# Optimization experiments

Measured on AMD Instinct MI355X. Metric: run time of the kernel, lower is better.

## Reference

```python
import jax, jax.numpy as jnp
import numpy as np

N = 524288
D_LATENT = 64


def _euler_to_quaternion(e):
    # e: [N,3] (roll, pitch, yaw). Mirrors euler_to_quaternion; stack order [qx,qy,qz,qw].
    r, p, y = e[:, 0] * 0.5, e[:, 1] * 0.5, e[:, 2] * 0.5
    sr, cr = jnp.sin(r), jnp.cos(r)
    sp, cp = jnp.sin(p), jnp.cos(p)
    sy, cy = jnp.sin(y), jnp.cos(y)
    qx = sr * cp * cy - cr * sp * sy
    qy = cr * sp * cy + sr * cp * sy
    qz = cr * cp * sy - sr * sp * cy
    qw = cr * cp * cy + sr * sp * sy
    return jnp.stack([qx, qy, qz, qw], axis=-1)  # [N,4]


def _compute_rot_mats(rot):
    # rot: [N,3] azimuth/elevation/theta in radians. Mirrors compute_RotMats (degree=False).
    a = -rot[:, 0]
    e = jnp.pi / 2.0 + rot[:, 1]
    t = -rot[:, 2]
    sa, ca = jnp.sin(a), jnp.cos(a)
    se, ce = jnp.sin(e), jnp.cos(e)
    st, ct = jnp.sin(t), jnp.cos(t)
    z = jnp.zeros_like(a)
    o = jnp.ones_like(a)
    Rz = jnp.stack([jnp.stack([ca, -sa, z], -1),
                    jnp.stack([sa, ca, z], -1),
                    jnp.stack([z, z, o], -1)], -2)   # [N,3,3]
    Rx = jnp.stack([jnp.stack([o, z, z], -1),
                    jnp.stack([z, ce, -se], -1),
                    jnp.stack([z, se, ce], -1)], -2)
    Rz2 = jnp.stack([jnp.stack([ct, -st, z], -1),
                     jnp.stack([st, ct, z], -1),
                     jnp.stack([z, z, o], -1)], -2)
    return jnp.einsum('nij,njk,nkl->nil', Rz2, Rx, Rz)  # [N,3,3]


def setup_inputs() -> dict:
    key = jax.random.key(0)
    k = jax.random.split(key, 6)
    return {
        'pose_pred': jax.random.uniform(k[0], (N, 3), dtype=jnp.float32),
        'pose_gt': jax.random.uniform(k[1], (N, 3), dtype=jnp.float32),
        'trans_pred': jax.random.normal(k[2], (N, 3), dtype=jnp.float32),
        'trans_gt': jax.random.normal(k[3], (N, 3), dtype=jnp.float32),
        'latent_pred': jax.random.normal(k[4], (N, D_LATENT), dtype=jnp.float32),
        'latent_gt': jax.random.normal(k[5], (N, D_LATENT), dtype=jnp.float32),
    }


def reference(pose_pred, pose_gt, trans_pred, trans_gt, latent_pred, latent_gt):
    # category='laptop' -> symm=False (no zeroing of elevation column)
    pp = pose_pred * jnp.pi
    pg = pose_gt * jnp.pi

    # rot_loss: MSE between quaternions (compute_quat_loss)
    rot_loss = jnp.mean((_euler_to_quaternion(pp) - _euler_to_quaternion(pg)) ** 2)

    # trans_loss / latent_loss: plain MSE (compute_l2_loss)
    trans_loss = jnp.mean((trans_pred - trans_gt) ** 2)
    latent_loss = jnp.mean((latent_pred - latent_gt) ** 2)

    # rot_distance: geodesic angle in degrees (rot_error, fully vectorized over batch)
    Rp = _compute_rot_mats(pp)
    Rg = _compute_rot_mats(pg)
    tr = jnp.einsum('nij,nij->n', Rp, Rg)  # trace(Rp @ Rg^T)
    rot_distance = jnp.arccos(jnp.clip((tr - 1.0) * 0.5, -1.0, 1.0)) * (180.0 / jnp.pi)  # [N]

    # trans_distance (trans_error)
    tp = trans_pred[:, 0:1] * trans_pred[:, 1:3]
    tg = trans_gt[:, 0:1] * trans_gt[:, 1:3]
    trans_distance = jnp.linalg.norm(tg - tp, axis=1) * 100.0  # [N]

    return (rot_loss, trans_loss, latent_loss, rot_distance, trans_distance)
```

## Files before the change

kernel.cpp:

```cpp
#include <hip/hip_runtime.h>
#include <math.h>

constexpr int NROWS = 524288;
constexpr float PI_F = 3.14159265358979323846f;
constexpr int BLOCK = 256;
constexpr int PA_BLOCKS = 512;
constexpr int TOTAL_BLOCKS = 2048;
constexpr int NL4 = NROWS * 64 / 4;
constexpr int CA = 2560;
constexpr int CB = 4608;


__device__ __forceinline__ void rot_mat(float r0, float r1, float r2, float R[9]) {
    float sa, ca, se, ce, st, ct;
    __sincosf(-r0, &sa, &ca);
    __sincosf(1.57079632679489662f + r1, &se, &ce);
    __sincosf(-r2, &st, &ct);
    R[0] =  ct * ca - st * ce * sa;
    R[1] = -ct * sa - st * ce * ca;
    R[2] =  st * se;
    R[3] =  st * ca + ct * ce * sa;
    R[4] = -st * sa + ct * ce * ca;
    R[5] = -ct * se;
    R[6] =  se * sa;
    R[7] =  se * ca;
    R[8] =  ce;
}

__device__ __forceinline__ void quat(float x0, float x1, float x2, float q[4]) {
    float sr, cr, sp, cp, sy, cy;
    __sincosf(x0 * 0.5f, &sr, &cr);
    __sincosf(x1 * 0.5f, &sp, &cp);
    __sincosf(x2 * 0.5f, &sy, &cy);
    q[0] = sr * cp * cy - cr * sp * sy;
    q[1] = cr * sp * cy + sr * cp * sy;
    q[2] = cr * cp * sy - sr * sp * cy;
    q[3] = cr * cp * cy + sr * sp * sy;
}

__device__ __forceinline__ void latent_chunk(
    const float4* __restrict__ lp, const float4* __restrict__ lg,
    int start, int count_per_thread, int tix, float& s2)
{
    int i = start + tix;
    for (int j = 0; j < count_per_thread; j += 2, i += 2 * BLOCK) {
        float4 p0 = lp[i],         g0 = lg[i];
        float4 p1 = lp[i + BLOCK], g1 = lg[i + BLOCK];
        float e;
        e = p0.x - g0.x; s2 += e * e;
        e = p0.y - g0.y; s2 += e * e;
        e = p0.z - g0.z; s2 += e * e;
        e = p0.w - g0.w; s2 += e * e;
        e = p1.x - g1.x; s2 += e * e;
        e = p1.y - g1.y; s2 += e * e;
        e = p1.z - g1.z; s2 += e * e;
        e = p1.w - g1.w; s2 += e * e;
    }
}

__global__ __launch_bounds__(256) void crit_fused_kernel(
    const float* __restrict__ pose_pred, const float* __restrict__ pose_gt,
    const float* __restrict__ trans_pred, const float* __restrict__ trans_gt,
    const float* __restrict__ latent_pred, const float* __restrict__ latent_gt,
    float* __restrict__ out, float* __restrict__ part)
{
    float s0 = 0.0f, s1 = 0.0f, s2 = 0.0f;
    const int b = blockIdx.x;
    const int tix = threadIdx.x;
    const float4* __restrict__ lp = reinterpret_cast<const float4*>(latent_pred);
    const float4* __restrict__ lg = reinterpret_cast<const float4*>(latent_gt);

    if (b < PA_BLOCKS) {
        const int t = b * BLOCK + tix;
        {
            const float4* pp4 = reinterpret_cast<const float4*>(pose_pred);
            const float4* pg4 = reinterpret_cast<const float4*>(pose_gt);
            float4 A0 = pp4[3*t+0], A1 = pp4[3*t+1], A2 = pp4[3*t+2];
            float4 B0 = pg4[3*t+0], B1 = pg4[3*t+1], B2 = pg4[3*t+2];
            float pp[12] = {A0.x,A0.y,A0.z,A0.w, A1.x,A1.y,A1.z,A1.w, A2.x,A2.y,A2.z,A2.w};
            float pg[12] = {B0.x,B0.y,B0.z,B0.w, B1.x,B1.y,B1.z,B1.w, B2.x,B2.y,B2.z,B2.w};
            #pragma unroll
            for (int r = 0; r < 4; ++r) {
                float x0 = pp[3*r]*PI_F, x1 = pp[3*r+1]*PI_F, x2 = pp[3*r+2]*PI_F;
                float y0 = pg[3*r]*PI_F, y1 = pg[3*r+1]*PI_F, y2 = pg[3*r+2]*PI_F;
                float qp[4], qg[4];
                quat(x0, x1, x2, qp);
                quat(y0, y1, y2, qg);
                #pragma unroll
                for (int k = 0; k < 4; ++k) { float d = qp[k] - qg[k]; s0 += d * d; }
                float Rp[9], Rg[9];
                rot_mat(x0, x1, x2, Rp);
                rot_mat(y0, y1, y2, Rg);
                float tr = 0.0f;
                #pragma unroll
                for (int k = 0; k < 9; ++k) tr += Rp[k] * Rg[k];
                float c = fminf(1.0f, fmaxf(-1.0f, (tr - 1.0f) * 0.5f));
                out[3 + 4*t + r] = acosf(c) * (180.0f / PI_F);
            }
        }
        {
            const float4* tp4 = reinterpret_cast<const float4*>(trans_pred);
            const float4* tg4 = reinterpret_cast<const float4*>(trans_gt);
            float4 C0 = tp4[3*t+0], C1 = tp4[3*t+1], C2 = tp4[3*t+2];
            float4 D0 = tg4[3*t+0], D1 = tg4[3*t+1], D2 = tg4[3*t+2];
            float tp[12] = {C0.x,C0.y,C0.z,C0.w, C1.x,C1.y,C1.z,C1.w, C2.x,C2.y,C2.z,C2.w};
            float tg[12] = {D0.x,D0.y,D0.z,D0.w, D1.x,D1.y,D1.z,D1.w, D2.x,D2.y,D2.z,D2.w};
            #pragma unroll
            for (int r = 0; r < 4; ++r) {
                float p0 = tp[3*r], p1 = tp[3*r+1], p2 = tp[3*r+2];
                float g0 = tg[3*r], g1 = tg[3*r+1], g2 = tg[3*r+2];
                float d0 = p0-g0, d1 = p1-g1, d2 = p2-g2;
                s1 += d0*d0 + d1*d1 + d2*d2;
                float a1 = g0*g1 - p0*p1;
                float a2 = g0*g2 - p0*p2;
                out[3 + NROWS + 4*t + r] = sqrtf(a1*a1 + a2*a2) * 100.0f;
            }
        }
        latent_chunk(lp, lg, b * CA, CA / BLOCK, tix, s2);
    } else {
        const int start = PA_BLOCKS * CA + (b - PA_BLOCKS) * CB;
        latent_chunk(lp, lg, start, CB / BLOCK, tix, s2);
    }

    #pragma unroll
    for (int off = 32; off > 0; off >>= 1) {
        s0 += __shfl_down(s0, off, 64);
        s1 += __shfl_down(s1, off, 64);
        s2 += __shfl_down(s2, off, 64);
    }
    __shared__ float sp[3][4];
    const int lane = threadIdx.x & 63;
    const int wave = threadIdx.x >> 6;
    if (lane == 0) { sp[0][wave] = s0; sp[1][wave] = s1; sp[2][wave] = s2; }
    __syncthreads();
    if (threadIdx.x == 0) {
        part[0*TOTAL_BLOCKS + b] = sp[0][0] + sp[0][1] + sp[0][2] + sp[0][3];
        part[1*TOTAL_BLOCKS + b] = sp[1][0] + sp[1][1] + sp[1][2] + sp[1][3];
        part[2*TOTAL_BLOCKS + b] = sp[2][0] + sp[2][1] + sp[2][2] + sp[2][3];
    }
}

__global__ __launch_bounds__(256) void finalize_kernel(
    const float* __restrict__ part, float* __restrict__ out)
{
    double a0 = 0.0, a1 = 0.0, a2 = 0.0;
    for (int j = threadIdx.x; j < TOTAL_BLOCKS; j += BLOCK) {
        a0 += (double)part[0*TOTAL_BLOCKS + j];
        a1 += (double)part[1*TOTAL_BLOCKS + j];
        a2 += (double)part[2*TOTAL_BLOCKS + j];
    }
    #pragma unroll
    for (int off = 32; off > 0; off >>= 1) {
        a0 += __shfl_down(a0, off, 64);
        a1 += __shfl_down(a1, off, 64);
        a2 += __shfl_down(a2, off, 64);
    }
    __shared__ double sp[3][4];
    const int lane = threadIdx.x & 63;
    const int wave = threadIdx.x >> 6;
    if (lane == 0) { sp[0][wave] = a0; sp[1][wave] = a1; sp[2][wave] = a2; }
    __syncthreads();
    if (threadIdx.x == 0) {
        double r = sp[0][0] + sp[0][1] + sp[0][2] + sp[0][3];
        double t = sp[1][0] + sp[1][1] + sp[1][2] + sp[1][3];
        double l = sp[2][0] + sp[2][1] + sp[2][2] + sp[2][3];
        out[0] = (float)(r / (4.0  * NROWS));
        out[1] = (float)(t / (3.0  * NROWS));
        out[2] = (float)(l / (64.0 * NROWS));
    }
}

extern "C" void kernel_launch(void* const* d_in, const int* in_sizes, int n_in,
                              void* d_out, int out_size, void* d_ws, size_t ws_size,
                              hipStream_t stream) {
    const float* pose_pred   = (const float*)d_in[0];
    const float* pose_gt     = (const float*)d_in[1];
    const float* trans_pred  = (const float*)d_in[2];
    const float* trans_gt    = (const float*)d_in[3];
    const float* latent_pred = (const float*)d_in[4];
    const float* latent_gt   = (const float*)d_in[5];
    float* out  = (float*)d_out;
    float* part = (float*)d_ws;

    hipLaunchKernelGGL(crit_fused_kernel, dim3(TOTAL_BLOCKS), dim3(BLOCK), 0, stream,
                       pose_pred, pose_gt, trans_pred, trans_gt,
                       latent_pred, latent_gt, out, part);
    hipLaunchKernelGGL(finalize_kernel, dim3(1), dim3(BLOCK), 0, stream, part, out);
}
```

Baseline: 51.52 us.

## Replace finalize kernel with last-block atomic reduction and deepen latent unroll

Removes the separate single-block finalize kernel. Each block now atomically adds its partial sums into double accumulators and bumps a counter, and the last block to arrive writes the final means. The workspace is zeroed with a memset before launch. The latent-only blocks also unroll to four float4 pairs per iteration for more loads in flight. This trades a kernel launch for a memset plus 2048 contended double atomics, and the summation order becomes nondeterministic.

Result: slower. 149.9 us (+190.9%).

```diff
diff --git a/kernel.cpp b/kernel.cpp
--- a/kernel.cpp
+++ b/kernel.cpp
@@ -6,7 +6,6 @@
 constexpr int BLOCK = 256;
 constexpr int PA_BLOCKS = 512;
 constexpr int TOTAL_BLOCKS = 2048;
-constexpr int NL4 = NROWS * 64 / 4;
 constexpr int CA = 2560;
 constexpr int CB = 4608;
 
@@ -38,7 +37,15 @@
     q[3] = cr * cp * cy + sr * sp * sy;
 }
 
-__device__ __forceinline__ void latent_chunk(
+__device__ __forceinline__ void lat_pair(const float4& p, const float4& g, float& s2) {
+    float e;
+    e = p.x - g.x; s2 += e * e;
+    e = p.y - g.y; s2 += e * e;
+    e = p.z - g.z; s2 += e * e;
+    e = p.w - g.w; s2 += e * e;
+}
+
+__device__ __forceinline__ void latent_chunk2(
     const float4* __restrict__ lp, const float4* __restrict__ lg,
     int start, int count_per_thread, int tix, float& s2)
 {
@@ -46,15 +53,32 @@
     for (int j = 0; j < count_per_thread; j += 2, i += 2 * BLOCK) {
         float4 p0 = lp[i],         g0 = lg[i];
         float4 p1 = lp[i + BLOCK], g1 = lg[i + BLOCK];
-        float e;
-        e = p0.x - g0.x; s2 += e * e;
-        e = p0.y - g0.y; s2 += e * e;
-        e = p0.z - g0.z; s2 += e * e;
-        e = p0.w - g0.w; s2 += e * e;
-        e = p1.x - g1.x; s2 += e * e;
-        e = p1.y - g1.y; s2 += e * e;
-        e = p1.z - g1.z; s2 += e * e;
-        e = p1.w - g1.w; s2 += e * e;
+        lat_pair(p0, g0, s2);
+        lat_pair(p1, g1, s2);
+    }
+}
+
+__device__ __forceinline__ void latent_chunk4(
+    const float4* __restrict__ lp, const float4* __restrict__ lg,
+    int start, int count_per_thread, int tix, float& s2)
+{
+    int i = start + tix;
+    int j = 0;
+    for (; j + 4 <= count_per_thread; j += 4, i += 4 * BLOCK) {
+        float4 p0 = lp[i],             g0 = lg[i];
+        float4 p1 = lp[i +     BLOCK], g1 = lg[i +     BLOCK];
+        float4 p2 = lp[i + 2 * BLOCK], g2 = lg[i + 2 * BLOCK];
+        float4 p3 = lp[i + 3 * BLOCK], g3 = lg[i + 3 * BLOCK];
+        lat_pair(p0, g0, s2);
+        lat_pair(p1, g1, s2);
+        lat_pair(p2, g2, s2);
+        lat_pair(p3, g3, s2);
+    }
+    for (; j < count_per_thread; j += 2, i += 2 * BLOCK) {
+        float4 p0 = lp[i],         g0 = lg[i];
+        float4 p1 = lp[i + BLOCK], g1 = lg[i + BLOCK];
+        lat_pair(p0, g0, s2);
+        lat_pair(p1, g1, s2);
     }
 }
 
@@ -62,7 +86,7 @@
     const float* __restrict__ pose_pred, const float* __restrict__ pose_gt,
     const float* __restrict__ trans_pred, const float* __restrict__ trans_gt,
     const float* __restrict__ latent_pred, const float* __restrict__ latent_gt,
-    float* __restrict__ out, float* __restrict__ part)
+    float* __restrict__ out, double* __restrict__ acc, unsigned int* __restrict__ cnt)
 {
     float s0 = 0.0f, s1 = 0.0f, s2 = 0.0f;
     const int b = blockIdx.x;
@@ -116,10 +140,10 @@
                 out[3 + NROWS + 4*t + r] = sqrtf(a1*a1 + a2*a2) * 100.0f;
             }
         }
-        latent_chunk(lp, lg, b * CA, CA / BLOCK, tix, s2);
+        latent_chunk2(lp, lg, b * CA, CA / BLOCK, tix, s2);
     } else {
         const int start = PA_BLOCKS * CA + (b - PA_BLOCKS) * CB;
-        latent_chunk(lp, lg, start, CB / BLOCK, tix, s2);
+        latent_chunk4(lp, lg, start, CB / BLOCK, tix, s2);
     }
 
     #pragma unroll
@@ -133,40 +157,24 @@
     const int wave = threadIdx.x >> 6;
     if (lane == 0) { sp[0][wave] = s0; sp[1][wave] = s1; sp[2][wave] = s2; }
     __syncthreads();
+
     if (threadIdx.x == 0) {
-        part[0*TOTAL_BLOCKS + b] = sp[0][0] + sp[0][1] + sp[0][2] + sp[0][3];
-        part[1*TOTAL_BLOCKS + b] = sp[1][0] + sp[1][1] + sp[1][2] + sp[1][3];
-        part[2*TOTAL_BLOCKS + b] = sp[2][0] + sp[2][1] + sp[2][2] + sp[2][3];
-    }
-}
-
-__global__ __launch_bounds__(256) void finalize_kernel(
-    const float* __restrict__ part, float* __restrict__ out)
-{
-    double a0 = 0.0, a1 = 0.0, a2 = 0.0;
-    for (int j = threadIdx.x; j < TOTAL_BLOCKS; j += BLOCK) {
-        a0 += (double)part[0*TOTAL_BLOCKS + j];
-        a1 += (double)part[1*TOTAL_BLOCKS + j];
-        a2 += (double)part[2*TOTAL_BLOCKS + j];
-    }
-    #pragma unroll
-    for (int off = 32; off > 0; off >>= 1) {
-        a0 += __shfl_down(a0, off, 64);
-        a1 += __shfl_down(a1, off, 64);
-        a2 += __shfl_down(a2, off, 64);
-    }
-    __shared__ double sp[3][4];
-    const int lane = threadIdx.x & 63;
-    const int wave = threadIdx.x >> 6;
-    if (lane == 0) { sp[0][wave] = a0; sp[1][wave] = a1; sp[2][wave] = a2; }
-    __syncthreads();
-    if (threadIdx.x == 0) {
-        double r = sp[0][0] + sp[0][1] + sp[0][2] + sp[0][3];
-        double t = sp[1][0] + sp[1][1] + sp[1][2] + sp[1][3];
-        double l = sp[2][0] + sp[2][1] + sp[2][2] + sp[2][3];
-        out[0] = (float)(r / (4.0  * NROWS));
-        out[1] = (float)(t / (3.0  * NROWS));
-        out[2] = (float)(l / (64.0 * NROWS));
+        float rb = sp[0][0] + sp[0][1] + sp[0][2] + sp[0][3];
+        float tb = sp[1][0] + sp[1][1] + sp[1][2] + sp[1][3];
+        float lb = sp[2][0] + sp[2][1] + sp[2][2] + sp[2][3];
+        atomicAdd(&acc[0], (double)rb);
+        atomicAdd(&acc[1], (double)tb);
+        atomicAdd(&acc[2], (double)lb);
+        __threadfence();
+        unsigned int old = atomicAdd(cnt, 1u);
+        if (old == TOTAL_BLOCKS - 1) {
+            double r = atomicAdd(&acc[0], 0.0);
+            double t = atomicAdd(&acc[1], 0.0);
+            double l = atomicAdd(&acc[2], 0.0);
+            out[0] = (float)(r / (4.0  * NROWS));
+            out[1] = (float)(t / (3.0  * NROWS));
+            out[2] = (float)(l / (64.0 * NROWS));
+        }
     }
 }
 
@@ -179,11 +187,12 @@
     const float* trans_gt    = (const float*)d_in[3];
     const float* latent_pred = (const float*)d_in[4];
     const float* latent_gt   = (const float*)d_in[5];
-    float* out  = (float*)d_out;
-    float* part = (float*)d_ws;
+    float* out = (float*)d_out;
+    double* acc = (double*)d_ws;
+    unsigned int* cnt = (unsigned int*)((char*)d_ws + 24);
 
+    hipMemsetAsync(d_ws, 0, 32, stream);
     hipLaunchKernelGGL(crit_fused_kernel, dim3(TOTAL_BLOCKS), dim3(BLOCK), 0, stream,
                        pose_pred, pose_gt, trans_pred, trans_gt,
-                       latent_pred, latent_gt, out, part);
-    hipLaunchKernelGGL(finalize_kernel, dim3(1), dim3(BLOCK), 0, stream, part, out);
+                       latent_pred, latent_gt, out, acc, cnt);
 }
```
